# Kernel tuning notes

Measured on AMD Instinct MI355X. Metric: run time of the kernel, lower is better.

The kernel has to match this reference:

```python
import jax, jax.numpy as jnp
import numpy as np

B, CIN, COUT, GC, H, W = 8, 64, 64, 64, 320, 320
K = 3      # guided conv kernel size
P = 1      # padding
KGL = 3    # kernel-generation layer kernel size
LEAK = 0.2
EPS = 1e-5


def setup_inputs() -> dict:
    key = jax.random.key(0)
    ks = jax.random.split(key, 4)
    return {
        "data": jax.random.normal(ks[0], (B, CIN, H, W), jnp.float32),
        "guidance": jax.random.normal(ks[1], (B, GC, H, W), jnp.float32),
        "w_kgl": jax.random.normal(ks[2], (CIN, GC, KGL, KGL), jnp.float32) * 0.02,
        "b_kgl": jnp.zeros((CIN,), jnp.float32),
        "w_cc": jax.random.normal(ks[3], (CIN * COUT, GC), jnp.float32) * 0.02,
        "b_cc": jnp.zeros((CIN * COUT,), jnp.float32),
        "gamma": jnp.ones((COUT,), jnp.float32),
        "beta": jnp.zeros((COUT,), jnp.float32),
    }


def reference(data, guidance, w_kgl, b_kgl, w_cc, b_cc, gamma, beta):
    pad = P + KGL // 2  # = 2, so kernel map is [B, CIN, H+2P, W+2P]
    kernel = jax.lax.conv_general_dilated(
        guidance, w_kgl, window_strides=(1, 1),
        padding=[(pad, pad), (pad, pad)],
        dimension_numbers=("NCHW", "OIHW", "NCHW"),
    ) + b_kgl[None, :, None, None]

    # channel-wise guided conv: zero-pad input, multiply per-pixel kernel map,
    # then box-sum over KxK windows (== conv with an all-ones KxK kernel)
    xp = jnp.pad(data, ((0, 0), (0, 0), (P, P), (P, P)))  # [B,CIN,H+2P,W+2P]
    prod = xp * kernel
    x1 = jax.lax.reduce_window(prod, 0.0, jax.lax.add,
                               (1, 1, K, K), (1, 1, 1, 1), "VALID")  # [B,CIN,H,W]

    # cross-channel: per-frame 1x1 conv generated from mean guidance intensity
    mean_g = guidance.mean(axis=(2, 3))                       # [B, GC]
    kcc = (mean_g @ w_cc.T + b_cc).reshape(B, COUT, CIN)      # [B, Cout, Cin]
    x2 = jnp.einsum("bchw,boc->bohw", x1, kcc)                # [B, Cout, H, W]

    x3 = jnp.where(x2 > 0, x2, LEAK * x2)  # leaky relu

    # batchnorm (training-mode statistics over B,H,W per channel)
    mu = x3.mean(axis=(0, 2, 3), keepdims=True)
    var = x3.var(axis=(0, 2, 3), keepdims=True)
    xn = (x3 - mu) * jax.lax.rsqrt(var + EPS)
    return xn * gamma[None, :, None, None] + beta[None, :, None, None]
```

## Files before the change

kernel.cpp:

```cpp
#include <hip/hip_runtime.h>

#define BB 8
#define CINC 64
#define COUTC 64
#define GCC 64
#define HH 320
#define WW 320
#define HP 322
#define WP 322
#define LEAK 0.2f
#define EPSB 1e-5f
#define HWSZ (HH*WW)
#define HWPSZ (HP*WP)

typedef unsigned short u16;
typedef __attribute__((ext_vector_type(8))) short short8v;
typedef __attribute__((ext_vector_type(16))) float f32x16;
typedef __attribute__((ext_vector_type(4))) unsigned int u32x4;

static __device__ __forceinline__ u16 f2bf(float f) {
    unsigned u = __float_as_uint(f);
    u += 0x7fffu + ((u >> 16) & 1u);
    return (u16)(u >> 16);
}
static __device__ __forceinline__ unsigned pk2bf(float a, float b) {
    return (unsigned)f2bf(a) | ((unsigned)f2bf(b) << 16);
}
static __device__ __forceinline__ unsigned swzA(int cc) {
    return (unsigned)((((cc >> 1) & 1) << 5) | (((cc >> 2) & 1) << 4));
}
static __device__ __forceinline__ unsigned swzP(int px) {
    return ((unsigned)(px >> 2) & 7u) << 4;
}

__global__ __launch_bounds__(256) void k_mean(const float* __restrict__ g,
                                              float* __restrict__ mean_g) {
    int row = blockIdx.x;
    const float4* p = (const float4*)(g + (size_t)row * HWSZ);
    float s = 0.f;
    for (int i = threadIdx.x; i < HWSZ / 4; i += 256) {
        float4 v = p[i];
        s += v.x + v.y + v.z + v.w;
    }
    #pragma unroll
    for (int off = 32; off; off >>= 1) s += __shfl_down(s, off);
    __shared__ float ls[4];
    if ((threadIdx.x & 63) == 0) ls[threadIdx.x >> 6] = s;
    __syncthreads();
    if (threadIdx.x == 0)
        mean_g[row] = (ls[0] + ls[1] + ls[2] + ls[3]) * (1.f / (float)HWSZ);
}

__global__ __launch_bounds__(256) void k_kcc(const float* __restrict__ mean_g,
                                             const float* __restrict__ w_cc,
                                             const float* __restrict__ b_cc,
                                             u16* __restrict__ kccB) {
    int idx = blockIdx.x * 256 + threadIdx.x;
    if (idx >= BB * COUTC * CINC) return;
    int b = idx >> 12;
    int j = idx & 4095;
    const float* mg = mean_g + b * GCC;
    const float* wr = w_cc + (size_t)j * GCC;
    float s = b_cc[j];
    #pragma unroll
    for (int g = 0; g < GCC; ++g) s += mg[g] * wr[g];
    kccB[idx] = f2bf(s);
}

__global__ __launch_bounds__(256) void k_wb(const float* __restrict__ w_kgl,
                                            u16* __restrict__ wB) {
    int idx = blockIdx.x * 256 + threadIdx.x;
    if (idx >= 36864) return;
    int j   = idx & 7;
    int lhi = (idx >> 3) & 1;
    int l   = (idx >> 4) & 31;
    int nj  = (idx >> 9) & 1;
    int t   = idx >> 10;
    int tap = t % 9, gk = t / 9;
    int ks = gk & 1, gc = gk >> 1;
    int cout = nj * 32 + l;
    int g = gc * 32 + ks * 16 + lhi * 8 + j;
    wB[idx] = f2bf(w_kgl[((size_t)(cout * 64 + g)) * 9 + tap]);
}

__global__ __launch_bounds__(384) void k_convm(const float* __restrict__ guid,
                                               const u16* __restrict__ wB,
                                               const float* __restrict__ b_kgl,
                                               u16* __restrict__ ker, int b0) {
    int xt = blockIdx.x, rt = blockIdx.y, bi = blockIdx.z;
    int bg = b0 + bi;
    int tid = threadIdx.x;
    int x0 = xt * 64, oy0 = rt * 6;
    __shared__ __align__(16) u16 ldsA[8 * 66 * 32];
    __shared__ __align__(16) u16 ldsB[9 * 2 * 32 * 16];

    int wv = tid >> 6, lane = tid & 63;
    int l31 = lane & 31, lhi = lane >> 5;
    f32x16 acc[2][2] = {};

    for (int gc = 0; gc < 2; ++gc) {
        for (int ks = 0; ks < 2; ++ks) {
            if (gc | ks) __syncthreads();
            const u16* bsrc = wB + (gc * 2 + ks) * 9216;
            #pragma unroll
            for (int k = 0; k < 3; ++k) {
                int i = tid + k * 384;
                *(u32x4*)(ldsB + (size_t)i * 8) = *(const u32x4*)(bsrc + (size_t)i * 8);
            }
            if (ks == 0) {
                const float* gbase = guid + ((size_t)bg * 64 + gc * 32) * HWSZ;
                for (int i = tid; i < 544; i += 384) {
                    int qa = i % 17;
                    int rem = i / 17;
                    int go = rem & 3, rr = rem >> 2;
                    int iy = oy0 - 2 + rr;
                    int ix0 = x0 - 4 + 4 * qa;
                    union { float4 q; float f[4]; } va[8];
                    bool rowok = (iy >= 0) & (iy < HH);
                    if (rowok & (ix0 >= 0) & (ix0 + 3 < WW)) {
                        #pragma unroll
                        for (int j = 0; j < 8; ++j)
                            va[j].q = *(const float4*)(gbase + (size_t)(go * 8 + j) * HWSZ
                                                       + (size_t)iy * WW + ix0);
                    } else {
                        #pragma unroll
                        for (int j = 0; j < 8; ++j)
                            #pragma unroll
                            for (int t = 0; t < 4; ++t) {
                                int ix = ix0 + t;
                                va[j].f[t] = (rowok & (ix >= 0) & (ix < WW))
                                    ? gbase[(size_t)(go * 8 + j) * HWSZ + (size_t)iy * WW + ix]
                                    : 0.f;
                            }
                    }
                    #pragma unroll
                    for (int t = 0; t < 4; ++t) {
                        int cc = 4 * qa - 2 + t;
                        if (cc >= 0 && cc < 66) {
                            u32x4 wvv;
                            wvv[0] = pk2bf(va[0].f[t], va[1].f[t]);
                            wvv[1] = pk2bf(va[2].f[t], va[3].f[t]);
                            wvv[2] = pk2bf(va[4].f[t], va[5].f[t]);
                            wvv[3] = pk2bf(va[6].f[t], va[7].f[t]);
                            unsigned off = ((unsigned)((rr * 66 + cc) * 4 + go) * 16u)
                                           ^ swzA(cc);
                            *(u32x4*)((char*)ldsA + off) = wvv;
                        }
                    }
                }
            }
            __syncthreads();

            for (int tap = 0; tap < 9; ++tap) {
                int di = tap / 3, dj = tap - di * 3;
                short8v Bf[2];
                #pragma unroll
                for (int nj = 0; nj < 2; ++nj)
                    Bf[nj] = *(const short8v*)(ldsB +
                        (((size_t)tap * 2 + nj) * 32 + l31) * 16 + lhi * 8);
                int rrow = wv + di;
                #pragma unroll
                for (int s = 0; s < 2; ++s) {
                    int cc = s * 32 + l31 + dj;
                    unsigned off = ((unsigned)((rrow * 66 + cc) * 4 + ks * 2 + lhi) * 16u)
                                   ^ swzA(cc);
                    short8v a = *(const short8v*)((const char*)ldsA + off);
                    acc[s][0] = __builtin_amdgcn_mfma_f32_32x32x16_bf16(a, Bf[0], acc[s][0], 0, 0, 0);
                    acc[s][1] = __builtin_amdgcn_mfma_f32_32x32x16_bf16(a, Bf[1], acc[s][1], 0, 0, 0);
                }
            }
        }
    }

    int oy = oy0 + wv;
    if (oy < HP) {
        float bias0 = b_kgl[l31], bias1 = b_kgl[32 + l31];
        u16* kout = ker + (size_t)bi * HWPSZ * GCC;
        int ckl = l31 >> 4, idx = l31 & 15;
        #pragma unroll
        for (int s = 0; s < 2; ++s)
            #pragma unroll
            for (int r = 0; r < 16; ++r) {
                int pxc = x0 + s * 32 + (r & 3) + 8 * (r >> 2) + 4 * lhi;
                if (pxc < WP) {
                    size_t pix = (size_t)oy * WP + pxc;
                    kout[((size_t)ckl * HWPSZ + pix) * 16 + idx]       = f2bf(acc[s][0][r] + bias0);
                    kout[((size_t)(2 + ckl) * HWPSZ + pix) * 16 + idx] = f2bf(acc[s][1][r] + bias1);
                }
            }
    }
}

__global__ __launch_bounds__(256) void k_mix(const float* __restrict__ data,
                                             const u16* __restrict__ ker,
                                             const u16* __restrict__ kccB,
                                             float* __restrict__ out,
                                             float* __restrict__ stats, int b0) {
    int xt = blockIdx.x, rt = blockIdx.y, bi = blockIdx.z;
    int b = b0 + bi;
    int w0 = xt * 64, oy0 = rt * 4;
    int tid = threadIdx.x, wv = tid >> 6, lane = tid & 63;
    int l31 = lane & 31, lhi = lane >> 5;

    __shared__ __align__(16) float prd[2 * 396 * 8];
    __shared__ float bsum[64], bsq[64];

    if (tid < 64) { bsum[tid] = 0.f; bsq[tid] = 0.f; }

    const u16* kerb = ker + (size_t)bi * HWPSZ * GCC;
    const float* datb = data + (size_t)b * CINC * HWSZ;
    const u16* kcb  = kccB + (size_t)b * COUTC * CINC;

    f32x16 acc[2][2] = {};
    float pvr[4][8];

#define MIX_LOAD(CK)                                                          \
    {                                                                         \
        _Pragma("unroll")                                                     \
        for (int it = 0; it < 4; ++it) {                                      \
            int t = tid + it * 256;                                           \
            if (t < 792) {                                                    \
                int c2 = t >= 396 ? 1 : 0;                                    \
                int px = t - c2 * 396;                                        \
                int r = px / 66, cc = px - r * 66;                            \
                int u = oy0 + r, kcol = w0 + cc;                              \
                int iu = u - 1, iv = kcol - 1;                                \
                _Pragma("unroll")                                             \
                for (int j = 0; j < 8; ++j) pvr[it][j] = 0.f;                 \
                if (u < HP && iu >= 0 && iu < HH && iv >= 0 && iv < WW) {     \
                    u32x4 kz = *(const u32x4*)(kerb + ((size_t)(CK) * HWPSZ + (size_t)u * WP + kcol) * 16 + c2 * 8); \
                    const float* dp = datb + ((size_t)(CK) * 16 + c2 * 8) * HWSZ + (size_t)iu * WW + iv; \
                    _Pragma("unroll")                                         \
                    for (int p = 0; p < 4; ++p) {                             \
                        pvr[it][2 * p]     = __uint_as_float(kz[p] << 16) * dp[(size_t)(2 * p) * HWSZ];       \
                        pvr[it][2 * p + 1] = __uint_as_float(kz[p] & 0xffff0000u) * dp[(size_t)(2 * p + 1) * HWSZ]; \
                    }                                                         \
                }                                                             \
            }                                                                 \
        }                                                                     \
    }

    MIX_LOAD(0);

    #pragma unroll
    for (int ck = 0; ck < 4; ++ck) {
        if (ck) __syncthreads();
        #pragma unroll
        for (int it = 0; it < 4; ++it) {
            int t = tid + it * 256;
            if (t < 792) {
                int c2 = t >= 396 ? 1 : 0;
                int px = t - c2 * 396;
                unsigned fo = (unsigned)((c2 * 3168 + px * 8) * 4);
                unsigned x = swzP(px);
                *(float4*)((char*)prd + (fo ^ x))        = make_float4(pvr[it][0], pvr[it][1], pvr[it][2], pvr[it][3]);
                *(float4*)((char*)prd + ((fo + 16) ^ x)) = make_float4(pvr[it][4], pvr[it][5], pvr[it][6], pvr[it][7]);
            }
        }
        __syncthreads();
        if (ck < 3) MIX_LOAD(ck + 1);

        short8v ka0 = *(const short8v*)(kcb + ((size_t)l31 * 64 + ck * 16 + lhi * 8));
        short8v ka1 = *(const short8v*)(kcb + ((size_t)(32 + l31) * 64 + ck * 16 + lhi * 8));

        #pragma unroll
        for (int s = 0; s < 2; ++s) {
            float x1v[8];
            #pragma unroll
            for (int j = 0; j < 8; ++j) x1v[j] = 0.f;
            #pragma unroll
            for (int di = 0; di < 3; ++di) {
                int row = wv + di;
                #pragma unroll
                for (int dj = 0; dj < 3; ++dj) {
                    int col = s * 32 + l31 + dj;
                    int px = row * 66 + col;
                    unsigned fo = (unsigned)((lhi * 3168 + px * 8) * 4);
                    unsigned x = swzP(px);
                    float4 a0 = *(const float4*)((const char*)prd + (fo ^ x));
                    float4 a1 = *(const float4*)((const char*)prd + ((fo + 16) ^ x));
                    x1v[0] += a0.x; x1v[1] += a0.y; x1v[2] += a0.z; x1v[3] += a0.w;
                    x1v[4] += a1.x; x1v[5] += a1.y; x1v[6] += a1.z; x1v[7] += a1.w;
                }
            }
            union { u16 h[8]; short8v v8; } xb;
            #pragma unroll
            for (int j = 0; j < 8; ++j) xb.h[j] = f2bf(x1v[j]);
            acc[0][s] = __builtin_amdgcn_mfma_f32_32x32x16_bf16(ka0, xb.v8, acc[0][s], 0, 0, 0);
            acc[1][s] = __builtin_amdgcn_mfma_f32_32x32x16_bf16(ka1, xb.v8, acc[1][s], 0, 0, 0);
        }
    }
#undef MIX_LOAD

    int oy = oy0 + wv;
    if (oy < HH) {
        #pragma unroll
        for (int nj = 0; nj < 2; ++nj)
            #pragma unroll
            for (int r = 0; r < 16; ++r) {
                int o = nj * 32 + (r & 3) + 8 * (r >> 2) + 4 * lhi;
                float v0 = acc[nj][0][r]; v0 = v0 > 0.f ? v0 : LEAK * v0;
                float v1 = acc[nj][1][r]; v1 = v1 > 0.f ? v1 : LEAK * v1;
                size_t rowb = ((size_t)(b * COUTC + o)) * HWSZ + (size_t)oy * WW + w0;
                out[rowb + l31]      = v0;
                out[rowb + 32 + l31] = v1;
                float ss = v0 + v1, qq = v0 * v0 + v1 * v1;
                #pragma unroll
                for (int off = 16; off; off >>= 1) {
                    ss += __shfl_xor(ss, off);
                    qq += __shfl_xor(qq, off);
                }
                if (l31 == 0) { atomicAdd(&bsum[o], ss); atomicAdd(&bsq[o], qq); }
            }
    }
    __syncthreads();
    int rep = (blockIdx.x + blockIdx.y * 5 + blockIdx.z * 3) & 7;
    if (tid < 64) {
        atomicAdd(&stats[rep * 128 + tid], bsum[tid]);
        atomicAdd(&stats[rep * 128 + 64 + tid], bsq[tid]);
    }
}

__global__ void k_fin(const float* __restrict__ stats,
                      const float* __restrict__ gamma, const float* __restrict__ beta,
                      float* __restrict__ scale, float* __restrict__ shift) {
    int o = threadIdx.x;
    float s = 0.f, q = 0.f;
    #pragma unroll
    for (int r = 0; r < 8; ++r) { s += stats[r * 128 + o]; q += stats[r * 128 + 64 + o]; }
    float n = (float)BB * (float)HWSZ;
    float mu = s / n;
    float var = q / n - mu * mu;
    float rs = rsqrtf(var + EPSB);
    float sc = rs * gamma[o];
    scale[o] = sc;
    shift[o] = beta[o] - mu * sc;
}

__global__ __launch_bounds__(256) void k_norm(float* __restrict__ x,
                                              const float* __restrict__ scale,
                                              const float* __restrict__ shift) {
    size_t i = (size_t)blockIdx.x * 256 + threadIdx.x;
    int ch = (int)((i * 4) / HWSZ) & 63;
    float4 v = ((float4*)x)[i];
    float sc = scale[ch], sh = shift[ch];
    v.x = v.x * sc + sh; v.y = v.y * sc + sh; v.z = v.z * sc + sh; v.w = v.w * sc + sh;
    ((float4*)x)[i] = v;
}

extern "C" void kernel_launch(void* const* d_in, const int* in_sizes, int n_in,
                              void* d_out, int out_size, void* d_ws, size_t ws_size,
                              hipStream_t stream) {
    const float* data  = (const float*)d_in[0];
    const float* guid  = (const float*)d_in[1];
    const float* w_kgl = (const float*)d_in[2];
    const float* b_kgl = (const float*)d_in[3];
    const float* w_cc  = (const float*)d_in[4];
    const float* b_cc  = (const float*)d_in[5];
    const float* gamma = (const float*)d_in[6];
    const float* beta  = (const float*)d_in[7];
    float* out = (float*)d_out;
    float* ws  = (float*)d_ws;

    float* mean_g = ws;
    float* stats  = ws + 512;
    float* scale  = stats + 1024;
    float* shift  = scale + 64;
    u16*   kccB   = (u16*)(ws + 1664);
    u16*   wB     = kccB + BB * 4096;
    u16*   kerC   = wB + 36864;

    size_t used_us = 1664 * 2 + BB * 4096 + 36864;
    size_t cap_us  = (ws_size / 2 > used_us) ? ws_size / 2 - used_us : 0;
    size_t per_b   = (size_t)HWPSZ * GCC;
    int bs = 8;
    while (bs > 1 && (size_t)bs * per_b > cap_us) bs >>= 1;

    hipMemsetAsync(stats, 0, 1024 * sizeof(float), stream);
    k_mean<<<BB * GCC, 256, 0, stream>>>(guid, mean_g);
    k_kcc<<<(BB * COUTC * CINC + 255) / 256, 256, 0, stream>>>(mean_g, w_cc, b_cc, kccB);
    k_wb<<<144, 256, 0, stream>>>(w_kgl, wB);

    for (int b0 = 0; b0 < BB; b0 += bs) {
        int nb = (BB - b0 < bs) ? BB - b0 : bs;
        k_convm<<<dim3(6, 54, nb), 384, 0, stream>>>(guid, wB, b_kgl, kerC, b0);
        k_mix<<<dim3(5, 80, nb), 256, 0, stream>>>(data, kerC, kccB, out, stats, b0);
    }
    k_fin<<<1, 64, 0, stream>>>(stats, gamma, beta, scale, shift);
    k_norm<<<(out_size / 4 + 255) / 256, 256, 0, stream>>>(out, scale, shift);
}
```

Measured before the change: 551.8 us.

## Pre-sum vertical taps in registers before LDS in guided-conv mix kernel

```diff
diff --git a/kernel.cpp b/kernel.cpp
--- a/kernel.cpp
+++ b/kernel.cpp
@@ -29,9 +29,10 @@
 static __device__ __forceinline__ unsigned swzA(int cc) {
     return (unsigned)((((cc >> 1) & 1) << 5) | (((cc >> 2) & 1) << 4));
 }
-static __device__ __forceinline__ unsigned swzP(int px) {
-    return ((unsigned)(px >> 2) & 7u) << 4;
-}
+static __device__ __forceinline__ unsigned swz2(int px, int c2) {
+    return (unsigned)((((px >> 2) + (c2 << 2)) & 7) << 4);
+}
+#define VST 2176
 
 __global__ __launch_bounds__(256) void k_mean(const float* __restrict__ g,
                                               float* __restrict__ mean_g) {
@@ -202,7 +203,7 @@
     int tid = threadIdx.x, wv = tid >> 6, lane = tid & 63;
     int l31 = lane & 31, lhi = lane >> 5;
 
-    __shared__ __align__(16) float prd[2 * 396 * 8];
+    __shared__ __align__(16) float prd[2 * VST];
     __shared__ float bsum[64], bsq[64];
 
     if (tid < 64) { bsum[tid] = 0.f; bsq[tid] = 0.f; }
@@ -212,28 +213,58 @@
     const u16* kcb  = kccB + (size_t)b * COUTC * CINC;
 
     f32x16 acc[2][2] = {};
-    float pvr[4][8];
+    float vs[4][8];
+
+    int uu = tid;
+    int c2u = uu & 1;
+    int rw = uu >> 1;
+    int orow = rw / 17;
+    int winu = rw - orow * 17;
+    int col0 = winu * 4;
+    int iv0 = w0 + col0 - 1;
+    bool colfast = (winu < 16) & (iv0 >= 0);
 
 #define MIX_LOAD(CK)                                                          \
-    {                                                                         \
+    if (uu < 136) {                                                           \
         _Pragma("unroll")                                                     \
-        for (int it = 0; it < 4; ++it) {                                      \
-            int t = tid + it * 256;                                           \
-            if (t < 792) {                                                    \
-                int c2 = t >= 396 ? 1 : 0;                                    \
-                int px = t - c2 * 396;                                        \
-                int r = px / 66, cc = px - r * 66;                            \
-                int u = oy0 + r, kcol = w0 + cc;                              \
-                int iu = u - 1, iv = kcol - 1;                                \
-                _Pragma("unroll")                                             \
-                for (int j = 0; j < 8; ++j) pvr[it][j] = 0.f;                 \
-                if (u < HP && iu >= 0 && iu < HH && iv >= 0 && iv < WW) {     \
-                    u32x4 kz = *(const u32x4*)(kerb + ((size_t)(CK) * HWPSZ + (size_t)u * WP + kcol) * 16 + c2 * 8); \
-                    const float* dp = datb + ((size_t)(CK) * 16 + c2 * 8) * HWSZ + (size_t)iu * WW + iv; \
+        for (int t = 0; t < 4; ++t)                                           \
+            _Pragma("unroll")                                                 \
+            for (int j = 0; j < 8; ++j) vs[t][j] = 0.f;                       \
+        _Pragma("unroll")                                                     \
+        for (int di = 0; di < 3; ++di) {                                      \
+            int uk = oy0 + orow + di;              \
+            int iu = uk - 1;                                                  \
+            if (iu >= 0 && iu < HH) {                                         \
+                if (colfast) {                                                \
+                    union { float4 q; float f[4]; } dq[8];                    \
+                    const float* dp = datb + ((size_t)(CK) * 16 + c2u * 8) * HWSZ \
+                                      + (size_t)iu * WW + iv0;                \
                     _Pragma("unroll")                                         \
-                    for (int p = 0; p < 4; ++p) {                             \
-                        pvr[it][2 * p]     = __uint_as_float(kz[p] << 16) * dp[(size_t)(2 * p) * HWSZ];       \
-                        pvr[it][2 * p + 1] = __uint_as_float(kz[p] & 0xffff0000u) * dp[(size_t)(2 * p + 1) * HWSZ]; \
+                    for (int j = 0; j < 8; ++j) dq[j].q = *(const float4*)(dp + (size_t)j * HWSZ); \
+                    const u16* kp = kerb + ((size_t)(CK) * HWPSZ + (size_t)uk * WP + w0 + col0) * 16 + c2u * 8; \
+                    _Pragma("unroll")                                         \
+                    for (int t = 0; t < 4; ++t) {                             \
+                        u32x4 kz = *(const u32x4*)(kp + t * 16);              \
+                        _Pragma("unroll")                                     \
+                        for (int p = 0; p < 4; ++p) {                         \
+                            vs[t][2 * p]     += __uint_as_float(kz[p] << 16) * dq[2 * p].f[t]; \
+                            vs[t][2 * p + 1] += __uint_as_float(kz[p] & 0xffff0000u) * dq[2 * p + 1].f[t]; \
+                        }                                                     \
+                    }                                                         \
+                } else {                                                      \
+                    _Pragma("unroll")                                         \
+                    for (int t = 0; t < 4; ++t) {                             \
+                        int cc = col0 + t;                                    \
+                        int iv = w0 + cc - 1;                                 \
+                        if (cc < 66 && iv >= 0 && iv < WW) {                  \
+                            u32x4 kz = *(const u32x4*)(kerb + ((size_t)(CK) * HWPSZ + (size_t)uk * WP + w0 + cc) * 16 + c2u * 8); \
+                            const float* dp2 = datb + ((size_t)(CK) * 16 + c2u * 8) * HWSZ + (size_t)iu * WW + iv; \
+                            _Pragma("unroll")                                 \
+                            for (int p = 0; p < 4; ++p) {                     \
+                                vs[t][2 * p]     += __uint_as_float(kz[p] << 16) * dp2[(size_t)(2 * p) * HWSZ];       \
+                                vs[t][2 * p + 1] += __uint_as_float(kz[p] & 0xffff0000u) * dp2[(size_t)(2 * p + 1) * HWSZ]; \
+                            }                                                 \
+                        }                                                     \
                     }                                                         \
                 }                                                             \
             }                                                                 \
@@ -245,16 +276,14 @@
     #pragma unroll
     for (int ck = 0; ck < 4; ++ck) {
         if (ck) __syncthreads();
-        #pragma unroll
-        for (int it = 0; it < 4; ++it) {
-            int t = tid + it * 256;
-            if (t < 792) {
-                int c2 = t >= 396 ? 1 : 0;
-                int px = t - c2 * 396;
-                unsigned fo = (unsigned)((c2 * 3168 + px * 8) * 4);
-                unsigned x = swzP(px);
-                *(float4*)((char*)prd + (fo ^ x))        = make_float4(pvr[it][0], pvr[it][1], pvr[it][2], pvr[it][3]);
-                *(float4*)((char*)prd + ((fo + 16) ^ x)) = make_float4(pvr[it][4], pvr[it][5], pvr[it][6], pvr[it][7]);
+        if (uu < 136) {
+            int px0 = orow * 68 + col0;
+            unsigned x = swz2(px0, c2u);
+            #pragma unroll
+            for (int t = 0; t < 4; ++t) {
+                unsigned fo = (unsigned)((c2u * VST + (px0 + t) * 8) * 4);
+                *(float4*)((char*)prd + (fo ^ x))        = make_float4(vs[t][0], vs[t][1], vs[t][2], vs[t][3]);
+                *(float4*)((char*)prd + ((fo + 16) ^ x)) = make_float4(vs[t][4], vs[t][5], vs[t][6], vs[t][7]);
             }
         }
         __syncthreads();
@@ -269,19 +298,15 @@
             #pragma unroll
             for (int j = 0; j < 8; ++j) x1v[j] = 0.f;
             #pragma unroll
-            for (int di = 0; di < 3; ++di) {
-                int row = wv + di;
-                #pragma unroll
-                for (int dj = 0; dj < 3; ++dj) {
-                    int col = s * 32 + l31 + dj;
-                    int px = row * 66 + col;
-                    unsigned fo = (unsigned)((lhi * 3168 + px * 8) * 4);
-                    unsigned x = swzP(px);
-                    float4 a0 = *(const float4*)((const char*)prd + (fo ^ x));
-                    float4 a1 = *(const float4*)((const char*)prd + ((fo + 16) ^ x));
-                    x1v[0] += a0.x; x1v[1] += a0.y; x1v[2] += a0.z; x1v[3] += a0.w;
-                    x1v[4] += a1.x; x1v[5] += a1.y; x1v[6] += a1.z; x1v[7] += a1.w;
-                }
+            for (int dj = 0; dj < 3; ++dj) {
+                int col = s * 32 + l31 + dj;
+                int px = wv * 68 + col;
+                unsigned fo = (unsigned)((lhi * VST + px * 8) * 4);
+                unsigned x = swz2(px, lhi);
+                float4 a0 = *(const float4*)((const char*)prd + (fo ^ x));
+                float4 a1 = *(const float4*)((const char*)prd + ((fo + 16) ^ x));
+                x1v[0] += a0.x; x1v[1] += a0.y; x1v[2] += a0.z; x1v[3] += a0.w;
+                x1v[4] += a1.x; x1v[5] += a1.y; x1v[6] += a1.z; x1v[7] += a1.w;
             }
             union { u16 h[8]; short8v v8; } xb;
             #pragma unroll
```

After: 628.4 us. 1.14x slower.
